# Performance work log

Measured on AMD Instinct MI355X. Metric: run time of the kernel, lower is better.

## Reference

```python
import jax, jax.numpy as jnp
import numpy as np

D_MODEL, D_INNER, D_STATE, DT_RANK, D_CONV = 192, 384, 16, 12, 4
DEPTH, HP, NHEADS, BATCH = 24, 14, 3, 4
EPS = 1e-5

def _make_rope():
    half = D_MODEL // 2
    fb = 1.0 / (10000.0 ** (np.arange(0, half, 2, dtype=np.float64) / half))
    t = np.arange(HP, dtype=np.float64)
    fr = np.repeat(np.outer(t, fb), 2, axis=-1)  # [14, 96]
    f = np.concatenate([np.broadcast_to(fr[:, None, :], (HP, HP, half)),
                        np.broadcast_to(fr[None, :, :], (HP, HP, half))], -1).reshape(HP * HP, D_MODEL)
    return jnp.asarray(np.cos(f), jnp.float32), jnp.asarray(np.sin(f), jnp.float32)

ROPE_COS, ROPE_SIN = _make_rope()

def _rotate_half(x):
    a, b = x[..., 0::2], x[..., 1::2]
    return jnp.stack([-b, a], axis=-1).reshape(x.shape)

def _apply_rope(h):
    # odd token count: cls token at position 0 is skipped (Vim behavior)
    sp = h[:, 1:, :]
    sp = sp * ROPE_COS + _rotate_half(sp) * ROPE_SIN
    return jnp.concatenate([h[:, :1, :], sp], axis=1)

def _rmsnorm(x, w):
    return x * jax.lax.rsqrt(jnp.mean(x * x, axis=-1, keepdims=True) + EPS) * w

def _scan_dir(u, z, cw, cb, xw, dw, db, alog, dp):
    # u, z: [B, L, d_inner]
    B, L, d = u.shape
    up = jnp.pad(u, ((0, 0), (D_CONV - 1, 0), (0, 0)))  # causal left pad
    xc = cb + sum(up[:, k:k + L, :] * cw[:, k] for k in range(D_CONV))
    x = jax.nn.silu(xc)
    dbl = x @ xw.T  # [B, L, dt_rank + 2*d_state]
    dt = dbl[..., :DT_RANK]
    Bm = dbl[..., DT_RANK:DT_RANK + D_STATE]
    C = dbl[..., DT_RANK + D_STATE:]
    delta = jax.nn.softplus(dt @ dw.T + db)  # [B, L, d]
    A = -jnp.exp(alog)  # [d, N]
    dA = jnp.exp(jnp.einsum('bld,dn->bldn', delta, A))
    dBu = jnp.einsum('bld,bln->bldn', delta * x, Bm)
    def step(h, inp):
        dA_t, dBu_t, C_t = inp
        h = dA_t * h + dBu_t
        return h, jnp.einsum('bdn,bn->bd', h, C_t)
    h0 = jnp.zeros((B, d, D_STATE), u.dtype)
    _, ys = jax.lax.scan(step, h0, (jnp.swapaxes(dA, 0, 1), jnp.swapaxes(dBu, 0, 1), jnp.swapaxes(C, 0, 1)))
    y = jnp.swapaxes(ys, 0, 1) + x * dp
    return y * jax.nn.silu(z)

def _mamba_bi(h, lp):
    nw, iw, cw, cb, xw, dw, db, alog, dp, ow = lp
    xz = h @ iw.T  # [B, L, 2*d_inner]
    x, z = xz[..., :D_INNER], xz[..., D_INNER:]
    yf = _scan_dir(x, z, cw[0], cb[0], xw[0], dw[0], db[0], alog[0], dp[0])
    yb = _scan_dir(x[:, ::-1], z[:, ::-1], cw[1], cb[1], xw[1], dw[1], db[1], alog[1], dp[1])[:, ::-1]
    return ((yf + yb) @ ow.T) * 0.5  # if_devide_out=True

def _encoder(img, pw_, pb_, cls_, pos_, nw, iw, cw, cb, xw, dw, db, alog, dp, ow, nfw):
    B = img.shape[0]
    p = jax.lax.conv_general_dilated(img, pw_, (16, 16), 'VALID',
            dimension_numbers=('NCHW', 'OIHW', 'NCHW')) + pb_[None, :, None, None]
    tok = jnp.transpose(p.reshape(B, D_MODEL, HP * HP), (0, 2, 1))
    cls = jnp.broadcast_to(cls_[None, None, :], (B, 1, D_MODEL))
    h = jnp.concatenate([cls, tok], axis=1) + pos_
    def layer(carry, lp):
        hs, res = carry
        hs = _apply_rope(hs)
        res = hs + res  # fused add-norm, prenorm
        hs = _rmsnorm(res, lp[0])
        hs = _mamba_bi(hs, lp)
        return (hs, res), None
    (h, res), _ = jax.lax.scan(layer, (h, jnp.zeros_like(h)), (nw, iw, cw, cb, xw, dw, db, alog, dp, ow))
    h = _rmsnorm(h + res, nfw)  # final fused add-norm
    return jnp.transpose(h[:, 1:, :].reshape(B, HP, HP, D_MODEL), (0, 3, 1, 2))

def _dwconv3(x, w):
    return jax.lax.conv_general_dilated(x, w[:, None, :, :], (1, 1), 'SAME',
            dimension_numbers=('NCHW', 'OIHW', 'NCHW'), feature_group_count=D_MODEL)

def _cross_attention(qi, ki, vi, qw, qdw, kw, kdw, vw, vdw, pw, temp):
    q = _dwconv3(jnp.einsum('bchw,oc->bohw', qi, qw), qdw)
    k = _dwconv3(jnp.einsum('bchw,oc->bohw', ki, kw), kdw)
    v = _dwconv3(jnp.einsum('bchw,oc->bohw', vi, vw), vdw)
    B, C, H, W = q.shape
    c = C // NHEADS
    qh = q.reshape(B, NHEADS, c, H * W)
    kh = k.reshape(B, NHEADS, c, H * W)
    vh = v.reshape(B, NHEADS, c, H * W)
    qh = qh / jnp.maximum(jnp.linalg.norm(qh, axis=-1, keepdims=True), 1e-12)
    kh = kh / jnp.maximum(jnp.linalg.norm(kh, axis=-1, keepdims=True), 1e-12)
    attn = jax.nn.softmax(jnp.einsum('bhcn,bhdn->bhcd', qh, kh) * temp, axis=-1)
    out = jnp.einsum('bhcd,bhdn->bhcn', attn, vh).reshape(B, C, H, W)
    return jnp.einsum('bchw,oc->bohw', out, pw)

def setup_inputs() -> dict:
    key = jax.random.key(0)
    ks = jax.random.split(key, 24)
    r = lambda k, s, sc=0.02: sc * jax.random.normal(k, s, dtype=jnp.float32)
    return {
        'x1': jax.random.normal(ks[0], (BATCH, 3, 224, 224), dtype=jnp.float32),
        'x2': jax.random.normal(ks[1], (BATCH, 3, 224, 224), dtype=jnp.float32),
        'patch_w': r(ks[2], (2, D_MODEL, 3, 16, 16)),
        'patch_b': jnp.zeros((2, D_MODEL), jnp.float32),
        'cls_tok': r(ks[3], (2, D_MODEL)),
        'pos_embed': r(ks[4], (2, HP * HP + 1, D_MODEL)),
        'norm_w': jnp.ones((2, DEPTH, D_MODEL), jnp.float32),
        'in_w': r(ks[5], (2, DEPTH, 2 * D_INNER, D_MODEL)),
        'conv_w': r(ks[6], (2, DEPTH, 2, D_INNER, D_CONV), 0.2),
        'conv_b': jnp.zeros((2, DEPTH, 2, D_INNER), jnp.float32),
        'xp_w': r(ks[7], (2, DEPTH, 2, DT_RANK + 2 * D_STATE, D_INNER)),
        'dt_w': r(ks[8], (2, DEPTH, 2, D_INNER, DT_RANK), 0.1),
        'dt_b': jnp.log(jnp.expm1(jax.random.uniform(ks[9], (2, DEPTH, 2, D_INNER), jnp.float32, 1e-3, 0.1))),
        'A_log': jnp.asarray(jnp.broadcast_to(jnp.log(jnp.arange(1.0, D_STATE + 1.0, dtype=jnp.float32)), (2, DEPTH, 2, D_INNER, D_STATE))),
        'Dp': jnp.ones((2, DEPTH, 2, D_INNER), jnp.float32),
        'out_w': r(ks[10], (2, DEPTH, D_MODEL, D_INNER)),
        'normf_w': jnp.ones((2, D_MODEL), jnp.float32),
        'qw': r(ks[11], (D_MODEL, D_MODEL)),
        'qdw': r(ks[12], (D_MODEL, 3, 3), 0.2),
        'kw': r(ks[13], (D_MODEL, D_MODEL)),
        'kdw': r(ks[14], (D_MODEL, 3, 3), 0.2),
        'vw': r(ks[15], (D_MODEL, D_MODEL)),
        'vdw': r(ks[16], (D_MODEL, 3, 3), 0.2),
        'pw': r(ks[17], (D_MODEL, D_MODEL)),
        'temp': jnp.ones((NHEADS, 1, 1), jnp.float32),
    }

def reference(x1, x2, patch_w, patch_b, cls_tok, pos_embed, norm_w, in_w, conv_w, conv_b, xp_w, dt_w, dt_b, A_log, Dp, out_w, normf_w, qw, qdw, kw, kdw, vw, vdw, pw, temp):
    f1 = _encoder(x1, patch_w[0], patch_b[0], cls_tok[0], pos_embed[0], norm_w[0], in_w[0], conv_w[0], conv_b[0], xp_w[0], dt_w[0], dt_b[0], A_log[0], Dp[0], out_w[0], normf_w[0])
    f2 = _encoder(x2, patch_w[1], patch_b[1], cls_tok[1], pos_embed[1], norm_w[1], in_w[1], conv_w[1], conv_b[1], xp_w[1], dt_w[1], dt_b[1], A_log[1], Dp[1], out_w[1], normf_w[1])
    return _cross_attention(f1, f2, f2, qw, qdw, kw, kdw, vw, vdw, pw, temp)
```

## Files before the change

### kernel.cpp

```cpp
#include <hip/hip_runtime.h>

#define DM 192
#define DI 384
#define DSt 16
#define DTR 12
#define DC 4
#define NL 24
#define HP 14
#define NH 3
#define NB 4
#define SL 197
#define NT 196
#define XZW 768
#define DBLW 44
#define TC 32
#define NCHK 7

static __device__ __forceinline__ float siluf(float x) { return x / (1.f + expf(-x)); }
static __device__ __forceinline__ float softplusf(float x) { return (x > 20.f) ? x : log1pf(expf(x)); }

template <int CTRL>
static __device__ __forceinline__ float dpp_addf(float x) {
  int y = __builtin_amdgcn_update_dpp(0, __float_as_int(x), CTRL, 0xF, 0xF, true);
  return x + __int_as_float(y);
}

static __device__ __forceinline__ float blk_sum3(float v, float* wsum) {
  for (int off = 32; off; off >>= 1) v += __shfl_xor(v, off, 64);
  int wid = threadIdx.x >> 6;
  if ((threadIdx.x & 63) == 0) wsum[wid] = v;
  __syncthreads();
  return wsum[0] + wsum[1] + wsum[2];
}
static __device__ __forceinline__ float blk_sum4(float v, float* wsum) {
  for (int off = 32; off; off >>= 1) v += __shfl_xor(v, off, 64);
  int wid = threadIdx.x >> 6;
  if ((threadIdx.x & 63) == 0) wsum[wid] = v;
  __syncthreads();
  return wsum[0] + wsum[1] + wsum[2] + wsum[3];
}

__global__ void k_rope_init(float* __restrict__ cosT, float* __restrict__ sinT) {
  int gid = blockIdx.x * blockDim.x + threadIdx.x;
  if (gid >= NT * DM) return;
  int c = gid % DM, tk = gid / DM;
  int py = tk / HP, px = tk % HP;
  int pos = (c < 96) ? py : px;
  int i = (c < 96) ? (c >> 1) : ((c - 96) >> 1);
  double fb = pow(10000.0, -((double)(2 * i)) / 96.0);
  double ang = (double)pos * fb;
  cosT[gid] = (float)cos(ang);
  sinT[gid] = (float)sin(ang);
}

__global__ void k_im2col(const float* __restrict__ x1, const float* __restrict__ x2,
                         float* __restrict__ P) {
  int gid = blockIdx.x * blockDim.x + threadIdx.x;
  if (gid >= 2 * 784 * 768) return;
  int col = gid % 768;
  int row = (gid / 768) % 784;
  int e = gid / (768 * 784);
  int b = row / NT, tk = row % NT;
  int c = col >> 8, r = (col >> 4) & 15, xx = col & 15;
  int py = tk / HP, px = tk % HP;
  const float* img = e ? x2 : x1;
  P[gid] = img[((size_t)(b * 3 + c) * 224 + (py * 16 + r)) * 224 + (px * 16 + xx)];
}

__global__ void k_patch_fin(const float* __restrict__ pm, const float* __restrict__ pb,
                            const float* __restrict__ cls, const float* __restrict__ pos,
                            float* __restrict__ h, float* __restrict__ res) {
  int gid = blockIdx.x * blockDim.x + threadIdx.x;
  if (gid >= 2 * NB * SL * DM) return;
  int c = gid % DM;
  int t = (gid / DM) % SL;
  int b = (gid / (DM * SL)) % NB;
  int e = gid / (DM * SL * NB);
  float v;
  if (t == 0) v = cls[e * DM + c];
  else v = pm[((size_t)e * 784 + b * NT + (t - 1)) * DM + c] + pb[e * DM + c];
  h[gid] = v + pos[((size_t)e * SL + t) * DM + c];
  res[gid] = 0.f;
}

__global__ __launch_bounds__(DM) void k_rope_res_norm(
    const float* __restrict__ h, float* __restrict__ res, float* __restrict__ hs,
    const float* __restrict__ nw, const float* __restrict__ cosT,
    const float* __restrict__ sinT, int l) {
  int bx = blockIdx.x;
  int t = bx % SL; int b = (bx / SL) % NB; int e = bx / (SL * NB);
  int c = threadIdx.x;
  __shared__ float sh[DM];
  __shared__ float wsum[3];
  size_t base = ((size_t)(e * NB + b) * SL + t) * DM;
  sh[c] = h[base + c];
  __syncthreads();
  float v = sh[c];
  if (t > 0) {
    int tk = t - 1;
    float co = cosT[tk * DM + c], si = sinT[tk * DM + c];
    float partner = sh[c ^ 1];
    float rot = (c & 1) ? partner : -partner;
    v = v * co + rot * si;
  }
  float r = res[base + c] + v;
  res[base + c] = r;
  float tot = blk_sum3(r * r, wsum);
  float scale = rsqrtf(tot / (float)DM + 1e-5f);
  hs[base + c] = r * scale * nw[(size_t)(e * NL + l) * DM + c];
}

struct MM4 {
  const float* A0[4];
  const float* A1[4];
  const float* B[4];
  float* C[4];
};
__global__ __launch_bounds__(256) void k_mm32(MM4 p, int M, int N, int K, float alpha) {
  const float* __restrict__ A0 = p.A0[blockIdx.z];
  const float* __restrict__ A1 = p.A1[blockIdx.z];
  const float* __restrict__ Bw = p.B[blockIdx.z];
  float* __restrict__ C = p.C[blockIdx.z];
  __shared__ __align__(16) float As[16][34];
  __shared__ __align__(16) float Bs[16][68];
  int tid = threadIdx.x;
  int m0 = blockIdx.y * 32, n0 = blockIdx.x * 64;
  int tm = tid >> 4, tn = tid & 15;
  int srow = tid >> 2, skq = tid & 3;
  int srowA = (tid & 127) >> 2;
  bool doA = tid < 128;
  int gmA = min(m0 + srowA, M - 1);
  int gnB = min(n0 + srow, N - 1);
  bool hasA1 = (A1 != nullptr);
  float4 ra, rb, ra1;

  auto GLOAD = [&](int k0) {
    if (doA) {
      ra = *(const float4*)&A0[(size_t)gmA * K + k0 + skq * 4];
      if (hasA1) ra1 = *(const float4*)&A1[(size_t)gmA * K + k0 + skq * 4];
    }
    rb = *(const float4*)&Bw[(size_t)gnB * K + k0 + skq * 4];
  };
  auto DSW = [&]() {
    int kb = skq * 4;
    if (doA) {
      float av0 = ra.x, av1 = ra.y, av2 = ra.z, av3 = ra.w;
      if (hasA1) { av0 += ra1.x; av1 += ra1.y; av2 += ra1.z; av3 += ra1.w; }
      As[kb + 0][srowA] = av0;
      As[kb + 1][srowA] = av1;
      As[kb + 2][srowA] = av2;
      As[kb + 3][srowA] = av3;
    }
    Bs[kb + 0][srow] = rb.x;
    Bs[kb + 1][srow] = rb.y;
    Bs[kb + 2][srow] = rb.z;
    Bs[kb + 3][srow] = rb.w;
  };

  float acc[2][4] = {};
  int T = K >> 4;
  GLOAD(0);
  DSW();
  __syncthreads();
#pragma unroll 1
  for (int kt = 1; kt <= T; ++kt) {
    if (kt < T) GLOAD(kt * 16);
#pragma unroll
    for (int kk = 0; kk < 16; ++kk) {
      float2 a = *(const float2*)&As[kk][tm * 2];
      float4 b = *(const float4*)&Bs[kk][tn * 4];
      acc[0][0] += a.x * b.x; acc[0][1] += a.x * b.y;
      acc[0][2] += a.x * b.z; acc[0][3] += a.x * b.w;
      acc[1][0] += a.y * b.x; acc[1][1] += a.y * b.y;
      acc[1][2] += a.y * b.z; acc[1][3] += a.y * b.w;
    }
    if (kt < T) {
      __syncthreads();
      DSW();
      __syncthreads();
    }
  }
#pragma unroll
  for (int mi = 0; mi < 2; ++mi) {
    int gm = m0 + tm * 2 + mi;
    if (gm >= M) continue;
    int gn = n0 + tn * 4;
    if (gn + 3 < N) {
      float4 o4 = make_float4(alpha * acc[mi][0], alpha * acc[mi][1],
                              alpha * acc[mi][2], alpha * acc[mi][3]);
      *(float4*)&C[(size_t)gm * N + gn] = o4;
    } else {
#pragma unroll
      for (int ni = 0; ni < 4; ++ni)
        if (gn + ni < N) C[(size_t)gm * N + gn + ni] = alpha * acc[mi][ni];
    }
  }
}

__global__ void k_conv_silu(const float* __restrict__ xz, const float* __restrict__ cw,
                            const float* __restrict__ cb, float* __restrict__ xs, int l) {
  int gid = blockIdx.x * blockDim.x + threadIdx.x;
  if (gid >= 2 * 2 * NB * SL * DI) return;
  int d = gid % DI;
  int t = (gid / DI) % SL;
  int b = (gid / (DI * SL)) % NB;
  int dir = (gid / (DI * SL * NB)) % 2;
  int e = gid / (DI * SL * NB * 2);
  size_t pidx = (size_t)(e * NL + l) * 2 + dir;
  const float* cwp = cw + (pidx * DI + d) * DC;
  float acc = cb[pidx * DI + d];
#pragma unroll
  for (int k = 0; k < DC; ++k) {
    int ts = t - (DC - 1) + k;
    if (ts >= 0) {
      int torig = dir ? (SL - 1 - ts) : ts;
      acc += cwp[k] * xz[((size_t)(e * NB + b) * SL + torig) * XZW + d];
    }
  }
  xs[gid] = siluf(acc);
}

__global__ void k_delta(const float* __restrict__ dbl, const float* __restrict__ dtw,
                        const float* __restrict__ dtb, float* __restrict__ delta, int l) {
  int gid = blockIdx.x * blockDim.x + threadIdx.x;
  if (gid >= 2 * 2 * NB * SL * DI) return;
  int d = gid % DI;
  int t = (gid / DI) % SL;
  int b = (gid / (DI * SL)) % NB;
  int dir = (gid / (DI * SL * NB)) % 2;
  int e = gid / (DI * SL * NB * 2);
  int z = e * 2 + dir;
  size_t pidx = (size_t)(e * NL + l) * 2 + dir;
  const float* row = dbl + ((size_t)(z * NB + b) * SL + t) * DBLW;
  const float* w = dtw + (pidx * DI + d) * DTR;
  float acc = dtb[pidx * DI + d];
#pragma unroll
  for (int r = 0; r < DTR; ++r) acc += row[r] * w[r];
  delta[gid] = softplusf(acc);
}

__global__ __launch_bounds__(256) void k_scan(
    const float* __restrict__ xs, const float* __restrict__ delta,
    const float* __restrict__ dbl, const float* __restrict__ xz,
    const float* __restrict__ alog, const float* __restrict__ dpw,
    float* __restrict__ y0, float* __restrict__ y1, int l) {
  int bx = blockIdx.x;
  int dg = bx % (DI / 16);
  int b = (bx / (DI / 16)) % NB;
  int dir = (bx / (DI / 16 * NB)) % 2;
  int e = bx / (DI / 16 * NB * 2);
  int tid = threadIdx.x;
  int n = tid & 15;
  int ch = tid >> 4;
  int d = dg * 16 + ch;
  size_t pidx = (size_t)(e * NL + l) * 2 + dir;
  float A = -expf(alog[(pidx * DI + d) * DSt + n]);
  float dpv = dpw[pidx * DI + d];
  int z = e * 2 + dir;
  size_t dblbase = ((size_t)(z * NB + b) * SL) * DBLW;
  float* yout = dir ? y1 : y0;
  size_t ybase = ((size_t)(e * NB + b) * SL) * DI + d;

  int lch = tid & 15;
  int ltt = tid >> 4;
  int lj = tid & 31;
  int ltt2 = tid >> 5;
  size_t gdbase = ((size_t)(z * NB + b) * SL) * DI + dg * 16 + lch;
  size_t gzbase = ((size_t)(e * NB + b) * SL) * XZW + DI + dg * 16 + lch;

  __shared__ float2 s_dx[2][TC][16];
  __shared__ float s_zv[2][TC][16];
  __shared__ float s_bc[2][TC][32];

  float r_dv[2], r_xv[2], r_zv[2], r_bc[4];

  auto LOADREG = [&](int c) {
    int t0 = c * TC;
#pragma unroll
    for (int k = 0; k < 2; ++k) {
      int t = t0 + ltt + 16 * k;
      int tm = t < SL ? t : SL - 1;
      r_dv[k] = delta[gdbase + (size_t)tm * DI];
      r_xv[k] = xs[gdbase + (size_t)tm * DI];
      int torig = dir ? (SL - 1 - tm) : tm;
      r_zv[k] = xz[gzbase + (size_t)torig * XZW];
    }
#pragma unroll
    for (int k = 0; k < 4; ++k) {
      int t = t0 + ltt2 + 8 * k;
      int tm = t < SL ? t : SL - 1;
      r_bc[k] = dbl[dblbase + (size_t)tm * DBLW + DTR + lj];
    }
  };
  auto STORE = [&](int pb) {
#pragma unroll
    for (int k = 0; k < 2; ++k) {
      s_dx[pb][ltt + 16 * k][lch] = make_float2(r_dv[k], r_xv[k]);
      s_zv[pb][ltt + 16 * k][lch] = r_zv[k];
    }
#pragma unroll
    for (int k = 0; k < 4; ++k) s_bc[pb][ltt2 + 8 * k][lj] = r_bc[k];
  };

  float hst = 0.f;
  auto COMP = [&](int pb, int c) {
    int t0 = c * TC;
#pragma unroll
    for (int half = 0; half < 2; ++half) {
      int i0 = half * 16;
      float ev[16], cc[16], cvv[16], xvv[16], pc[16];
#pragma unroll
      for (int i = 0; i < 16; ++i) {
        float2 dx = s_dx[pb][i0 + i][ch];
        float bm = s_bc[pb][i0 + i][n];
        xvv[i] = dx.y;
        cvv[i] = s_bc[pb][i0 + i][16 + n];
        ev[i] = __expf(dx.x * A);
        cc[i] = (dx.x * xvv[i]) * bm;
      }
#pragma unroll
      for (int i = 0; i < 16; ++i) {
        hst = ev[i] * hst + cc[i];
        pc[i] = hst * cvv[i];
      }
#pragma unroll
      for (int i = 0; i < 16; ++i) pc[i] = dpp_addf<0xB1>(pc[i]);
#pragma unroll
      for (int i = 0; i < 16; ++i) pc[i] = dpp_addf<0x4E>(pc[i]);
#pragma unroll
      for (int i = 0; i < 16; ++i) pc[i] = dpp_addf<0x114>(pc[i]);
#pragma unroll
      for (int i = 0; i < 16; ++i) pc[i] = dpp_addf<0x118>(pc[i]);
      if (n == 15) {
#pragma unroll
        for (int i = 0; i < 16; ++i) {
          int t = t0 + i0 + i;
          if (t < SL) {
            int torig = dir ? (SL - 1 - t) : t;
            float yv = pc[i] + xvv[i] * dpv;
            yout[ybase + (size_t)torig * DI] = yv * siluf(s_zv[pb][i0 + i][ch]);
          }
        }
      }
    }
  };

  LOADREG(0);
  STORE(0);
  LOADREG(1);
  __syncthreads();
  int pb = 0;
#pragma unroll 1
  for (int c = 0; c < NCHK; ++c) {
    COMP(pb, c);
    if (c + 1 < NCHK) {
      STORE(pb ^ 1);
      __syncthreads();
      if (c + 2 < NCHK) LOADREG(c + 2);
      pb ^= 1;
    }
  }
}

__global__ __launch_bounds__(DM) void k_final_norm(
    const float* __restrict__ h, const float* __restrict__ res,
    const float* __restrict__ nfw, float* __restrict__ fT) {
  int bx = blockIdx.x;
  int tk = bx % NT; int b = (bx / NT) % NB; int e = bx / (NT * NB);
  int c = threadIdx.x;
  __shared__ float wsum[3];
  size_t base = ((size_t)(e * NB + b) * SL + (tk + 1)) * DM;
  float r = h[base + c] + res[base + c];
  float tot = blk_sum3(r * r, wsum);
  float scale = rsqrtf(tot / (float)DM + 1e-5f);
  fT[((size_t)(e * NB + b) * NT + tk) * DM + c] = r * scale * nfw[e * DM + c];
}

__global__ void k_dwconv(const float* __restrict__ qkvl, const float* __restrict__ qdw,
                         const float* __restrict__ kdw, const float* __restrict__ vdw,
                         float* __restrict__ qkvd) {
  int gid = blockIdx.x * blockDim.x + threadIdx.x;
  if (gid >= 3 * NB * DM * NT) return;
  int nn = gid % NT;
  int o = (gid / NT) % DM;
  int b = (gid / (NT * DM)) % NB;
  int zz = gid / (NT * DM * NB);
  const float* wsel = (zz == 0 ? qdw : (zz == 1 ? kdw : vdw)) + o * 9;
  int y = nn / HP, x = nn % HP;
  const float* in = qkvl + ((size_t)zz * NB + b) * NT * DM;
  float acc = 0.f;
#pragma unroll
  for (int ky = 0; ky < 3; ++ky) {
    int yy = y + ky - 1;
    if (yy < 0 || yy >= HP) continue;
#pragma unroll
    for (int kx = 0; kx < 3; ++kx) {
      int xx = x + kx - 1;
      if (xx < 0 || xx >= HP) continue;
      acc += in[(size_t)(yy * HP + xx) * DM + o] * wsel[ky * 3 + kx];
    }
  }
  qkvd[gid] = acc;
}

__global__ __launch_bounds__(256) void k_l2norm(float* __restrict__ qkvd) {
  int bx = blockIdx.x;
  int C = bx % DM; int b = (bx / DM) % NB; int zz = bx / (DM * NB);
  int i = threadIdx.x;
  __shared__ float wsum[4];
  float* row = qkvd + ((size_t)zz * NB + b) * DM * NT + (size_t)C * NT;
  float v = (i < NT) ? row[i] : 0.f;
  float tot = blk_sum4(v * v, wsum);
  float sc = 1.f / fmaxf(sqrtf(tot), 1e-12f);
  if (i < NT) row[i] = v * sc;
}

__global__ __launch_bounds__(64) void k_attn_sm(const float* __restrict__ qkvd,
                                                const float* __restrict__ temp,
                                                float* __restrict__ P) {
  int bx = blockIdx.x;
  int i = bx % 64; int hh = (bx / 64) % NH; int b = bx / (64 * NH);
  int j = threadIdx.x;
  __shared__ float qs[NT];
  const float* qrow = qkvd + ((size_t)0 * NB + b) * DM * NT + (size_t)(hh * 64 + i) * NT;
  for (int k = j; k < NT; k += 64) qs[k] = qrow[k];
  __syncthreads();
  const float* krow = qkvd + ((size_t)1 * NB + b) * DM * NT + (size_t)(hh * 64 + j) * NT;
  float acc = 0.f;
  for (int k = 0; k < NT; ++k) acc += qs[k] * krow[k];
  acc *= temp[hh];
  float m = acc;
  for (int off = 32; off; off >>= 1) m = fmaxf(m, __shfl_xor(m, off, 64));
  float ex = expf(acc - m);
  float s = ex;
  for (int off = 32; off; off >>= 1) s += __shfl_xor(s, off, 64);
  P[((size_t)(b * NH + hh) * 64 + i) * 64 + j] = ex / s;
}

__global__ __launch_bounds__(256) void k_av(const float* __restrict__ P,
                                            const float* __restrict__ qkvd,
                                            float* __restrict__ att) {
  int bx = blockIdx.x;
  int i = bx % 64; int hh = (bx / 64) % NH; int b = bx / (64 * NH);
  int nn = threadIdx.x;
  __shared__ float ps[64];
  if (nn < 64) ps[nn] = P[((size_t)(b * NH + hh) * 64 + i) * 64 + nn];
  __syncthreads();
  if (nn >= NT) return;
  const float* vbase = qkvd + ((size_t)2 * NB + b) * DM * NT + (size_t)(hh * 64) * NT + nn;
  float acc = 0.f;
  for (int j = 0; j < 64; ++j) acc += ps[j] * vbase[(size_t)j * NT];
  att[((size_t)b * DM + hh * 64 + i) * NT + nn] = acc;
}

__global__ __launch_bounds__(256) void k_out(const float* __restrict__ att,
                                             const float* __restrict__ pw,
                                             float* __restrict__ out) {
  int bx = blockIdx.x;
  int o = bx % DM; int b = bx / DM;
  int nn = threadIdx.x;
  if (nn >= NT) return;
  const float* abase = att + (size_t)b * DM * NT + nn;
  const float* w = pw + (size_t)o * DM;
  float acc = 0.f;
  for (int c = 0; c < DM; ++c) acc += abase[(size_t)c * NT] * w[c];
  out[((size_t)b * DM + o) * NT + nn] = acc;
}

extern "C" void kernel_launch(void* const* d_in, const int* in_sizes, int n_in,
                              void* d_out, int out_size, void* d_ws, size_t ws_size,
                              hipStream_t stream) {
  const float* x1      = (const float*)d_in[0];
  const float* x2      = (const float*)d_in[1];
  const float* patch_w = (const float*)d_in[2];
  const float* patch_b = (const float*)d_in[3];
  const float* cls_tok = (const float*)d_in[4];
  const float* pos_emb = (const float*)d_in[5];
  const float* norm_w  = (const float*)d_in[6];
  const float* in_w    = (const float*)d_in[7];
  const float* conv_w  = (const float*)d_in[8];
  const float* conv_b  = (const float*)d_in[9];
  const float* xp_w    = (const float*)d_in[10];
  const float* dt_w    = (const float*)d_in[11];
  const float* dt_b    = (const float*)d_in[12];
  const float* A_log   = (const float*)d_in[13];
  const float* Dp      = (const float*)d_in[14];
  const float* out_w   = (const float*)d_in[15];
  const float* normf_w = (const float*)d_in[16];
  const float* qw      = (const float*)d_in[17];
  const float* qdw     = (const float*)d_in[18];
  const float* kw      = (const float*)d_in[19];
  const float* kdw     = (const float*)d_in[20];
  const float* vw      = (const float*)d_in[21];
  const float* vdw     = (const float*)d_in[22];
  const float* pww     = (const float*)d_in[23];
  const float* temp    = (const float*)d_in[24];

  float* ws = (float*)d_ws;
  size_t o = 0;
  float* cosT = ws + o; o += (size_t)NT * DM;
  float* sinT = ws + o; o += (size_t)NT * DM;
  float* hB   = ws + o; o += 2ull * NB * SL * DM;
  float* resB = ws + o; o += 2ull * NB * SL * DM;
  float* hsB  = ws + o; o += 2ull * NB * SL * DM;
  float* xzB  = ws + o; o += 2ull * NB * SL * XZW;
  float* xsB  = ws + o; o += 4ull * NB * SL * DI;
  float* dblB = ws + o; o += 4ull * NB * SL * DBLW;
  float* delB = ws + o; o += 4ull * NB * SL * DI;
  float* y0B  = ws + o; o += 2ull * NB * SL * DI;
  float* y1B  = ws + o; o += 2ull * NB * SL * DI;
  float* fTB  = ws + o; o += 2ull * NB * NT * DM;
  float* qkvL = ws + o; o += 3ull * NB * NT * DM;
  float* qkvD = ws + o; o += 3ull * NB * DM * NT;
  float* Pb   = ws + o; o += (size_t)NB * NH * 64 * 64;
  float* attB = ws + o; o += (size_t)NB * DM * NT;
  (void)ws_size; (void)in_sizes; (void)n_in; (void)out_size;

  const int M = NB * SL;

  k_rope_init<<<(NT * DM + 255) / 256, 256, 0, stream>>>(cosT, sinT);

  float* Pm = delB;
  float* Pout = y0B;
  k_im2col<<<(2 * 784 * 768 + 255) / 256, 256, 0, stream>>>(x1, x2, Pm);
  {
    MM4 p{};
    for (int e = 0; e < 2; ++e) {
      p.A0[e] = Pm + (size_t)e * 784 * 768;
      p.A1[e] = nullptr;
      p.B[e]  = patch_w + (size_t)e * DM * 768;
      p.C[e]  = Pout + (size_t)e * 784 * DM;
    }
    dim3 g((DM + 63) / 64, (784 + 31) / 32, 2);
    k_mm32<<<g, 256, 0, stream>>>(p, 784, DM, 768, 1.f);
  }
  k_patch_fin<<<(2 * NB * SL * DM + 255) / 256, 256, 0, stream>>>(
      Pout, patch_b, cls_tok, pos_emb, hB, resB);

  for (int l = 0; l < NL; ++l) {
    k_rope_res_norm<<<2 * NB * SL, DM, 0, stream>>>(hB, resB, hsB, norm_w, cosT, sinT, l);

    {
      MM4 p{};
      for (int e = 0; e < 2; ++e) {
        p.A0[e] = hsB + (size_t)e * M * DM;
        p.A1[e] = nullptr;
        p.B[e]  = in_w + (size_t)(e * NL + l) * XZW * DM;
        p.C[e]  = xzB + (size_t)e * M * XZW;
      }
      dim3 g((XZW + 63) / 64, (M + 31) / 32, 2);
      k_mm32<<<g, 256, 0, stream>>>(p, M, XZW, DM, 1.f);
    }

    k_conv_silu<<<(2 * 2 * NB * SL * DI + 255) / 256, 256, 0, stream>>>(xzB, conv_w, conv_b, xsB, l);

    {
      MM4 p{};
      for (int z = 0; z < 4; ++z) {
        int e = z / 2, dir = z % 2;
        p.A0[z] = xsB + (size_t)z * M * DI;
        p.A1[z] = nullptr;
        p.B[z]  = xp_w + ((size_t)(e * NL + l) * 2 + dir) * DBLW * DI;
        p.C[z]  = dblB + (size_t)z * M * DBLW;
      }
      dim3 g((DBLW + 63) / 64, (M + 31) / 32, 4);
      k_mm32<<<g, 256, 0, stream>>>(p, M, DBLW, DI, 1.f);
    }

    k_delta<<<(2 * 2 * NB * SL * DI + 255) / 256, 256, 0, stream>>>(dblB, dt_w, dt_b, delB, l);

    k_scan<<<2 * 2 * NB * (DI / 16), 256, 0, stream>>>(xsB, delB, dblB, xzB, A_log, Dp, y0B, y1B, l);

    {
      MM4 p{};
      for (int e = 0; e < 2; ++e) {
        p.A0[e] = y0B + (size_t)e * M * DI;
        p.A1[e] = y1B + (size_t)e * M * DI;
        p.B[e]  = out_w + (size_t)(e * NL + l) * DM * DI;
        p.C[e]  = hB + (size_t)e * M * DM;
      }
      dim3 g((DM + 63) / 64, (M + 31) / 32, 2);
      k_mm32<<<g, 256, 0, stream>>>(p, M, DM, DI, 0.5f);
    }
  }

  k_final_norm<<<2 * NB * NT, DM, 0, stream>>>(hB, resB, normf_w, fTB);

  {
    MM4 p{};
    const int Mq = NB * NT;
    p.A0[0] = fTB;                         p.A1[0] = nullptr; p.B[0] = qw; p.C[0] = qkvL;
    p.A0[1] = fTB + (size_t)NB * NT * DM;  p.A1[1] = nullptr; p.B[1] = kw; p.C[1] = qkvL + (size_t)Mq * DM;
    p.A0[2] = fTB + (size_t)NB * NT * DM;  p.A1[2] = nullptr; p.B[2] = vw; p.C[2] = qkvL + 2ull * Mq * DM;
    dim3 g((DM + 63) / 64, (Mq + 31) / 32, 3);
    k_mm32<<<g, 256, 0, stream>>>(p, Mq, DM, DM, 1.f);
  }

  k_dwconv<<<(3 * NB * DM * NT + 255) / 256, 256, 0, stream>>>(qkvL, qdw, kdw, vdw, qkvD);
  k_l2norm<<<2 * NB * DM, 256, 0, stream>>>(qkvD);
  k_attn_sm<<<NB * NH * 64, 64, 0, stream>>>(qkvD, temp, Pb);
  k_av<<<NB * NH * 64, 256, 0, stream>>>(Pb, qkvD, attB);
  k_out<<<NB * DM, 256, 0, stream>>>(attB, pww, (float*)d_out);
}
```

Measured before the change: 3.070 ms.

## Parallelize selective scan over time segments with two-pass chunked recurrence

Replaces the sequential 197-step scan per channel group with a chunked parallel scan. Each of four waves handles a 50-step segment: a first pass computes the local state and decay product, shared memory combines the segment carries, and a second pass recomputes with the correct initial state and writes outputs. The grid grows fourfold, with 4 channels per block instead of 16, to shorten the serial dependency chain. In exchange, the exp and loads are done twice, the LDS double-buffered staging is dropped in favour of direct global loads, and the output stores become more scattered.

```diff
diff --git a/kernel.cpp b/kernel.cpp
--- a/kernel.cpp
+++ b/kernel.cpp
@@ -13,8 +13,7 @@
 #define NT 196
 #define XZW 768
 #define DBLW 44
-#define TC 32
-#define NCHK 7
+#define SEG 50
 
 static __device__ __forceinline__ float siluf(float x) { return x / (1.f + expf(-x)); }
 static __device__ __forceinline__ float softplusf(float x) { return (x > 20.f) ? x : log1pf(expf(x)); }
@@ -245,119 +244,69 @@
     const float* __restrict__ alog, const float* __restrict__ dpw,
     float* __restrict__ y0, float* __restrict__ y1, int l) {
   int bx = blockIdx.x;
-  int dg = bx % (DI / 16);
-  int b = (bx / (DI / 16)) % NB;
-  int dir = (bx / (DI / 16 * NB)) % 2;
-  int e = bx / (DI / 16 * NB * 2);
+  int g4 = bx % (DI / 4);
+  int b = (bx / (DI / 4)) % NB;
+  int dir = (bx / (DI / 4 * NB)) % 2;
+  int e = bx / (DI / 4 * NB * 2);
   int tid = threadIdx.x;
-  int n = tid & 15;
-  int ch = tid >> 4;
-  int d = dg * 16 + ch;
+  int w = tid >> 6;
+  int lane = tid & 63;
+  int n = lane & 15;
+  int chl = lane >> 4;
+  int d = g4 * 4 + chl;
   size_t pidx = (size_t)(e * NL + l) * 2 + dir;
   float A = -expf(alog[(pidx * DI + d) * DSt + n]);
   float dpv = dpw[pidx * DI + d];
   int z = e * 2 + dir;
+  size_t gdbase = ((size_t)(z * NB + b) * SL) * DI + d;
   size_t dblbase = ((size_t)(z * NB + b) * SL) * DBLW;
+  size_t gzbase = ((size_t)(e * NB + b) * SL) * XZW + DI + d;
   float* yout = dir ? y1 : y0;
   size_t ybase = ((size_t)(e * NB + b) * SL) * DI + d;
 
-  int lch = tid & 15;
-  int ltt = tid >> 4;
-  int lj = tid & 31;
-  int ltt2 = tid >> 5;
-  size_t gdbase = ((size_t)(z * NB + b) * SL) * DI + dg * 16 + lch;
-  size_t gzbase = ((size_t)(e * NB + b) * SL) * XZW + DI + dg * 16 + lch;
-
-  __shared__ float2 s_dx[2][TC][16];
-  __shared__ float s_zv[2][TC][16];
-  __shared__ float s_bc[2][TC][32];
-
-  float r_dv[2], r_xv[2], r_zv[2], r_bc[4];
-
-  auto LOADREG = [&](int c) {
-    int t0 = c * TC;
-#pragma unroll
-    for (int k = 0; k < 2; ++k) {
-      int t = t0 + ltt + 16 * k;
-      int tm = t < SL ? t : SL - 1;
-      r_dv[k] = delta[gdbase + (size_t)tm * DI];
-      r_xv[k] = xs[gdbase + (size_t)tm * DI];
-      int torig = dir ? (SL - 1 - tm) : tm;
-      r_zv[k] = xz[gzbase + (size_t)torig * XZW];
-    }
-#pragma unroll
-    for (int k = 0; k < 4; ++k) {
-      int t = t0 + ltt2 + 8 * k;
-      int tm = t < SL ? t : SL - 1;
-      r_bc[k] = dbl[dblbase + (size_t)tm * DBLW + DTR + lj];
-    }
-  };
-  auto STORE = [&](int pb) {
-#pragma unroll
-    for (int k = 0; k < 2; ++k) {
-      s_dx[pb][ltt + 16 * k][lch] = make_float2(r_dv[k], r_xv[k]);
-      s_zv[pb][ltt + 16 * k][lch] = r_zv[k];
-    }
-#pragma unroll
-    for (int k = 0; k < 4; ++k) s_bc[pb][ltt2 + 8 * k][lj] = r_bc[k];
-  };
-
-  float hst = 0.f;
-  auto COMP = [&](int pb, int c) {
-    int t0 = c * TC;
-#pragma unroll
-    for (int half = 0; half < 2; ++half) {
-      int i0 = half * 16;
-      float ev[16], cc[16], cvv[16], xvv[16], pc[16];
-#pragma unroll
-      for (int i = 0; i < 16; ++i) {
-        float2 dx = s_dx[pb][i0 + i][ch];
-        float bm = s_bc[pb][i0 + i][n];
-        xvv[i] = dx.y;
-        cvv[i] = s_bc[pb][i0 + i][16 + n];
-        ev[i] = __expf(dx.x * A);
-        cc[i] = (dx.x * xvv[i]) * bm;
-      }
-#pragma unroll
-      for (int i = 0; i < 16; ++i) {
-        hst = ev[i] * hst + cc[i];
-        pc[i] = hst * cvv[i];
-      }
-#pragma unroll
-      for (int i = 0; i < 16; ++i) pc[i] = dpp_addf<0xB1>(pc[i]);
-#pragma unroll
-      for (int i = 0; i < 16; ++i) pc[i] = dpp_addf<0x4E>(pc[i]);
-#pragma unroll
-      for (int i = 0; i < 16; ++i) pc[i] = dpp_addf<0x114>(pc[i]);
-#pragma unroll
-      for (int i = 0; i < 16; ++i) pc[i] = dpp_addf<0x118>(pc[i]);
-      if (n == 15) {
-#pragma unroll
-        for (int i = 0; i < 16; ++i) {
-          int t = t0 + i0 + i;
-          if (t < SL) {
-            int torig = dir ? (SL - 1 - t) : t;
-            float yv = pc[i] + xvv[i] * dpv;
-            yout[ybase + (size_t)torig * DI] = yv * siluf(s_zv[pb][i0 + i][ch]);
-          }
-        }
-      }
-    }
-  };
-
-  LOADREG(0);
-  STORE(0);
-  LOADREG(1);
-  __syncthreads();
-  int pb = 0;
-#pragma unroll 1
-  for (int c = 0; c < NCHK; ++c) {
-    COMP(pb, c);
-    if (c + 1 < NCHK) {
-      STORE(pb ^ 1);
-      __syncthreads();
-      if (c + 2 < NCHK) LOADREG(c + 2);
-      pb ^= 1;
+  int t0 = w * SEG;
+  int t1 = min(SL, t0 + SEG);
+
+  float h = 0.f, ap = 1.f;
+#pragma unroll 2
+  for (int t = t0; t < t1; ++t) {
+    float dv = delta[gdbase + (size_t)t * DI];
+    float xv = xs[gdbase + (size_t)t * DI];
+    float bm = dbl[dblbase + (size_t)t * DBLW + DTR + n];
+    float a = __expf(dv * A);
+    h = a * h + (dv * xv) * bm;
+    ap *= a;
+  }
+
+  __shared__ float sh_h[4][64];
+  __shared__ float sh_a[4][64];
+  sh_h[w][lane] = h;
+  sh_a[w][lane] = ap;
+  __syncthreads();
+  float hin = 0.f;
+#pragma unroll
+  for (int j = 0; j < 3; ++j)
+    if (j < w) hin = sh_a[j][lane] * hin + sh_h[j][lane];
+
+  h = hin;
+#pragma unroll 2
+  for (int t = t0; t < t1; ++t) {
+    float dv = delta[gdbase + (size_t)t * DI];
+    float xv = xs[gdbase + (size_t)t * DI];
+    float bm = dbl[dblbase + (size_t)t * DBLW + DTR + n];
+    float cv = dbl[dblbase + (size_t)t * DBLW + DTR + DSt + n];
+    float a = __expf(dv * A);
+    h = a * h + (dv * xv) * bm;
+    float pc = h * cv;
+    pc = dpp_addf<0xB1>(pc);
+    pc = dpp_addf<0x4E>(pc);
+    pc = dpp_addf<0x114>(pc);
+    pc = dpp_addf<0x118>(pc);
+    if (n == 15) {
+      int torig = dir ? (SL - 1 - t) : t;
+      float zv = xz[gzbase + (size_t)torig * XZW];
+      float yv = pc + xv * dpv;
+      yout[ybase + (size_t)torig * DI] = yv * siluf(zv);
     }
   }
 }
@@ -569,7 +518,7 @@
 
     k_delta<<<(2 * 2 * NB * SL * DI + 255) / 256, 256, 0, stream>>>(dblB, dt_w, dt_b, delB, l);
 
-    k_scan<<<2 * 2 * NB * (DI / 16), 256, 0, stream>>>(xsB, delB, dblB, xzB, A_log, Dp, y0B, y1B, l);
+    k_scan<<<2 * 2 * NB * (DI / 4), 256, 0, stream>>>(xsB, delB, dblB, xzB, A_log, Dp, y0B, y1B, l);
 
     {
       MM4 p{};
```

Result: slower. 3.435 ms (+11.9%).
